# Kernel tuning notes

Measured on AMD Instinct MI355X. Metric: run time of the kernel, lower is better.

The kernel has to match this reference:

```python
import jax, jax.numpy as jnp
import numpy as np

D_MODEL = 2048
N_HEADS = 32
N_KV_HEADS = 8
HEAD_DIM = D_MODEL // N_HEADS  # 64
THETA = 10000.0
BATCH = 2
SEQ = 2048


def _rope_tables(seq_len, head_dim, theta):
    idx = jnp.arange(0, head_dim, 2, dtype=jnp.float32)
    inv_freq = 1.0 / (theta ** (idx / head_dim))
    pos = jnp.arange(seq_len, dtype=jnp.float32)
    angles = pos[:, None] * inv_freq[None, :]  # (S, head_dim/2)
    return jnp.cos(angles), jnp.sin(angles)


def _apply_rope(x, cos, sin):
    # x: (B, H, S, Dh); cos/sin: (S, Dh/2)
    c = cos[None, None, :, :]
    s = sin[None, None, :, :]
    x_even = x[..., 0::2]
    x_odd = x[..., 1::2]
    out_even = x_even * c - x_odd * s
    out_odd = x_even * s + x_odd * c
    # interleave back: stack on last axis and reshape
    return jnp.stack([out_even, out_odd], axis=-1).reshape(x.shape)


def setup_inputs() -> dict:
    key = jax.random.key(0)
    kx, kq, kk, kv, ko = jax.random.split(key, 5)
    std_sq = (2.0 / (D_MODEL + D_MODEL)) ** 0.5
    std_kv = (2.0 / (D_MODEL + N_KV_HEADS * HEAD_DIM)) ** 0.5
    return {
        "x": jax.random.normal(kx, (BATCH, SEQ, D_MODEL), dtype=jnp.float32),
        "Wq": jax.random.normal(kq, (D_MODEL, D_MODEL), dtype=jnp.float32) * std_sq,
        "Wk": jax.random.normal(kk, (N_KV_HEADS * HEAD_DIM, D_MODEL), dtype=jnp.float32) * std_kv,
        "Wv": jax.random.normal(kv, (N_KV_HEADS * HEAD_DIM, D_MODEL), dtype=jnp.float32) * std_kv,
        "Wo": jax.random.normal(ko, (D_MODEL, D_MODEL), dtype=jnp.float32) * std_sq,
    }


def reference(x, Wq, Wk, Wv, Wo):
    B, S, D = x.shape
    groups = N_HEADS // N_KV_HEADS
    cos, sin = _rope_tables(S, HEAD_DIM, THETA)

    q = (x @ Wq.T).reshape(B, S, N_HEADS, HEAD_DIM).transpose(0, 2, 1, 3)
    k = (x @ Wk.T).reshape(B, S, N_KV_HEADS, HEAD_DIM).transpose(0, 2, 1, 3)
    v = (x @ Wv.T).reshape(B, S, N_KV_HEADS, HEAD_DIM).transpose(0, 2, 1, 3)

    q = _apply_rope(q, cos, sin)
    k = _apply_rope(k, cos, sin)

    # GQA: repeat kv heads (repeat_interleave along head dim)
    k = jnp.repeat(k, groups, axis=1)  # (B, H, S, Dh)
    v = jnp.repeat(v, groups, axis=1)

    scale = 1.0 / jnp.sqrt(jnp.float32(HEAD_DIM))
    scores = jnp.einsum('bhqd,bhkd->bhqk', q, k) * scale
    causal = jnp.tril(jnp.ones((S, S), dtype=bool))
    scores = jnp.where(causal[None, None, :, :], scores, -jnp.inf)
    attn = jax.nn.softmax(scores, axis=-1)
    out = jnp.einsum('bhqk,bhkd->bhqd', attn, v)
    out = out.transpose(0, 2, 1, 3).reshape(B, S, D)
    return out @ Wo.T
```

## Files before the change

### kernel.cpp

```cpp
#include <hip/hip_runtime.h>
#include <math.h>

#define BATCHN 2
#define SEQ 2048
#define DMODEL 2048
#define NH 32
#define NKV 8
#define HDIM 64
#define KVD 512
#define ROWS 4096

typedef __bf16 bf16x8 __attribute__((ext_vector_type(8)));
typedef float f32x4 __attribute__((ext_vector_type(4)));
typedef unsigned short u16x8 __attribute__((ext_vector_type(8)));

#define MFMA(a, b, c) __builtin_amdgcn_mfma_f32_16x16x32_bf16(a, b, c, 0, 0, 0)

__device__ __forceinline__ unsigned short f2bf(float f) {
  union { float f; unsigned u; } v; v.f = f;
  unsigned u = v.u;
  u += 0x7fffu + ((u >> 16) & 1u);
  return (unsigned short)(u >> 16);
}

__device__ __forceinline__ unsigned cvtpk(float a, float b) {
  unsigned r;
  asm("v_cvt_pk_bf16_f32 %0, %1, %2" : "=v"(r) : "v"(a), "v"(b));
  return r;
}
__device__ __forceinline__ void pl32(unsigned& a, unsigned& b) {
  asm("v_permlane32_swap_b32 %0, %1" : "+v"(a), "+v"(b));
}
__device__ __forceinline__ void pl16(unsigned& a, unsigned& b) {
  asm("v_permlane16_swap_b32 %0, %1" : "+v"(a), "+v"(b));
}
__device__ __forceinline__ float exp2v(float x) {
  float r;
  asm("v_exp_f32 %0, %1" : "=v"(r) : "v"(x));
  return r;
}

__device__ __forceinline__ void gload16(const void* g, void* l) {
  __builtin_amdgcn_global_load_lds((const __attribute__((address_space(1))) unsigned int*)g,
                                   (__attribute__((address_space(3))) unsigned int*)l, 16, 0, 0);
}

#define FENCE() asm volatile("" ::: "memory")
#define BARRIER() do { FENCE(); __builtin_amdgcn_s_barrier(); FENCE(); } while (0)
#define VMCNT(n) asm volatile("s_waitcnt vmcnt(" #n ")" ::: "memory")

__global__ __launch_bounds__(256) void conv_all(const float* __restrict__ x,
                                                const float* __restrict__ Wq,
                                                const float* __restrict__ Wk,
                                                const float* __restrict__ Wv,
                                                const float* __restrict__ Wo,
                                                unsigned short* __restrict__ xb,
                                                unsigned short* __restrict__ Wqb,
                                                unsigned short* __restrict__ Wkb,
                                                unsigned short* __restrict__ Wvb,
                                                unsigned short* __restrict__ Wob,
                                                float* __restrict__ ct,
                                                float* __restrict__ st) {
  int i = blockIdx.x * 256 + threadIdx.x;
  const float* in;
  unsigned short* out;
  int off;
  if (i < 2097152)      { in = x;  out = xb;  off = i; }
  else if (i < 3145728) { in = Wq; out = Wqb; off = i - 2097152; }
  else if (i < 3407872) { in = Wk; out = Wkb; off = i - 3145728; }
  else if (i < 3670016) { in = Wv; out = Wvb; off = i - 3407872; }
  else if (i < 4718592) { in = Wo; out = Wob; off = i - 3670016; }
  else {
    int t = i - 4718592;
    int s = t >> 5, f = t & 31;
    float inv = __expf(-(float)f * (9.210340371976184f / 32.0f));
    float ang = (float)s * inv;
    ct[t] = cosf(ang);
    st[t] = sinf(ang);
    return;
  }
  float4 v = ((const float4*)in)[off];
  ushort4 o;
  o.x = f2bf(v.x); o.y = f2bf(v.y); o.z = f2bf(v.z); o.w = f2bf(v.w);
  ((ushort4*)out)[off] = o;
}

__global__ __launch_bounds__(512, 2) void gemm_qkv384(const unsigned short* __restrict__ A,
                                                      const unsigned short* __restrict__ Bq,
                                                      const unsigned short* __restrict__ Bk,
                                                      const unsigned short* __restrict__ Bv,
                                                      unsigned short* __restrict__ Qo,
                                                      unsigned short* __restrict__ Ko,
                                                      unsigned short* __restrict__ Vt,
                                                      const float* __restrict__ ct,
                                                      const float* __restrict__ st) {
  __shared__ __align__(16) unsigned short Als[3][8192];
  __shared__ __align__(16) unsigned short Bls[3][2][8192];
  const int tid = threadIdx.x, lane = tid & 63, wv = tid >> 6;
  const int wm = wv >> 2, wn = wv & 3;
  const int g = lane >> 4, r15 = lane & 15;
  const int c = blockIdx.x & 7, i = blockIdx.x >> 3;
  const int bm = (c >> 1) * 8 + (i & 7);
  const int grp = (c & 1) * 4 + (i >> 3);
  const int row0 = bm << 7;
  const unsigned short* Bpan[3];
  int bnp[3];
#pragma unroll
  for (int bk = 0; bk < 3; ++bk) {
    int p = grp * 3 + bk;
    bnp[bk] = p;
    Bpan[bk] = (p < 16) ? Bq + (size_t)(p << 7) * DMODEL
             : (p < 20) ? Bk + (size_t)((p - 16) << 7) * DMODEL
                        : Bv + (size_t)((p - 20) << 7) * DMODEL;
  }
  const int srow = tid >> 3;
  const int scol = (((tid & 7) ^ ((tid >> 3) & 7)) << 3);
  const unsigned short* gA = A + (size_t)(row0 + srow) * DMODEL + scol;
  const unsigned short* gB0 = Bpan[0] + (size_t)srow * DMODEL + scol;
  const unsigned short* gB1 = Bpan[1] + (size_t)srow * DMODEL + scol;
  const unsigned short* gB2 = Bpan[2] + (size_t)srow * DMODEL + scol;

  f32x4 acc[4][6];
#pragma unroll
  for (int a = 0; a < 4; ++a)
#pragma unroll
    for (int b = 0; b < 6; ++b) acc[a][b] = (f32x4){0.f, 0.f, 0.f, 0.f};

#define STG_A(buf, kt) do { \
    gload16(gA + (size_t)(kt) * 64, &Als[buf][(wv << 9)]); \
    gload16(gA + (size_t)64 * DMODEL + (size_t)(kt) * 64, &Als[buf][4096 + (wv << 9)]); } while (0)
#define STG_B(bank, gp, buf, kt) do { \
    gload16(gp + (size_t)(kt) * 64, &Bls[bank][buf][(wv << 9)]); \
    gload16(gp + (size_t)64 * DMODEL + (size_t)(kt) * 64, &Bls[bank][buf][4096 + (wv << 9)]); } while (0)
#define RA(buf, mf, kk) (*(const bf16x8*)&Als[buf][((wm << 6) + ((mf) << 4) + r15) * 64 + \
                          (((((kk) << 2) + g) ^ (r15 & 7)) << 3)])
#define RB(bank, buf, sub, kk) (*(const bf16x8*)&Bls[bank][buf][((wn << 5) + ((sub) << 4) + r15) * 64 + \
                          (((((kk) << 2) + g) ^ (r15 & 7)) << 3)])

  STG_A(0, 0);
  STG_B(0, gB0, 0, 0); STG_B(1, gB1, 0, 0); STG_B(2, gB2, 0, 0);
  STG_A(1, 1);
  VMCNT(0);
  BARRIER();

  const int NT = DMODEL / 64;
  for (int t = 0; t < NT; ++t) {
    const int ab = t % 3, an2 = (t + 2) % 3;
    const int bb = t & 1, bn2 = bb ^ 1;
    bf16x8 af[4][2];
#pragma unroll
    for (int mf = 0; mf < 4; ++mf) { af[mf][0] = RA(ab, mf, 0); af[mf][1] = RA(ab, mf, 1); }
    bf16x8 b01[2][2][2];
#pragma unroll
    for (int bk = 0; bk < 2; ++bk)
#pragma unroll
      for (int sub = 0; sub < 2; ++sub) {
        b01[bk][sub][0] = RB(bk, bb, sub, 0);
        b01[bk][sub][1] = RB(bk, bb, sub, 1);
      }
    if (t + 1 < NT) {
      STG_B(0, gB0, bn2, t + 1); STG_B(1, gB1, bn2, t + 1); STG_B(2, gB2, bn2, t + 1);
    }
    BARRIER();
    __builtin_amdgcn_s_setprio(1);
#pragma unroll
    for (int mf = 0; mf < 4; ++mf)
#pragma unroll
      for (int bk = 0; bk < 2; ++bk)
#pragma unroll
        for (int sub = 0; sub < 2; ++sub) {
          acc[mf][bk * 2 + sub] = MFMA(af[mf][0], b01[bk][sub][0], acc[mf][bk * 2 + sub]);
          acc[mf][bk * 2 + sub] = MFMA(af[mf][1], b01[bk][sub][1], acc[mf][bk * 2 + sub]);
        }
    __builtin_amdgcn_s_setprio(0);
    BARRIER();
    bf16x8 b2[2][2];
#pragma unroll
    for (int sub = 0; sub < 2; ++sub) { b2[sub][0] = RB(2, bb, sub, 0); b2[sub][1] = RB(2, bb, sub, 1); }
    if (t + 2 < NT) STG_A(an2, t + 2);
    BARRIER();
    __builtin_amdgcn_s_setprio(1);
#pragma unroll
    for (int mf = 0; mf < 4; ++mf)
#pragma unroll
      for (int sub = 0; sub < 2; ++sub) {
        acc[mf][4 + sub] = MFMA(af[mf][0], b2[sub][0], acc[mf][4 + sub]);
        acc[mf][4 + sub] = MFMA(af[mf][1], b2[sub][1], acc[mf][4 + sub]);
      }
    __builtin_amdgcn_s_setprio(0);
    if (t + 2 < NT)      { VMCNT(2); }
    else if (t + 1 < NT) { VMCNT(0); }
    BARRIER();
  }
#undef STG_A
#undef STG_B
#undef RA
#undef RB

  const float QS = 0.18033688011112042f;
#pragma unroll
  for (int bk = 0; bk < 3; ++bk) {
    const int p = bnp[bk];
    if (p < 20) {
      unsigned short* Outb = (p < 16) ? Qo : Ko;
      const int col0 = (p < 16) ? (p << 7) : ((p - 16) << 7);
      const int ldo = (p < 16) ? DMODEL : KVD;
      const int qsc = (p < 16);
#pragma unroll
      for (int mf = 0; mf < 4; ++mf) {
#pragma unroll
        for (int rr = 0; rr < 4; ++rr) {
          const int m = row0 + (wm << 6) + (mf << 4) + (g << 2) + rr;
          const float* ctr = ct + ((m & (SEQ - 1)) << 5);
          const float* str = st + ((m & (SEQ - 1)) << 5);
#pragma unroll
          for (int sub = 0; sub < 2; ++sub) {
            const int n = col0 + (wn << 5) + (sub << 4) + r15;
            float v = acc[mf][bk * 2 + sub][rr];
            float pv = __shfl_xor(v, 1);
            int fi = (n & 63) >> 1;
            float cc = ctr[fi], sn = str[fi];
            v = (lane & 1) ? (pv * sn + v * cc) : (v * cc - pv * sn);
            if (qsc) v *= QS;
            Outb[(size_t)m * ldo + n] = f2bf(v);
          }
        }
      }
    } else {
      const int col0 = (p - 20) << 7;
#pragma unroll
      for (int mf = 0; mf < 4; ++mf) {
        const int m0 = row0 + (wm << 6) + (mf << 4) + (g << 2);
        const int b = m0 >> 11, s0 = m0 & (SEQ - 1);
#pragma unroll
        for (int sub = 0; sub < 2; ++sub) {
          const int nv = col0 + (wn << 5) + (sub << 4) + r15;
          ushort4 o;
          o.x = f2bf(acc[mf][bk * 2 + sub][0]);
          o.y = f2bf(acc[mf][bk * 2 + sub][1]);
          o.z = f2bf(acc[mf][bk * 2 + sub][2]);
          o.w = f2bf(acc[mf][bk * 2 + sub][3]);
          *(ushort4*)(Vt + ((size_t)(b * NKV * HDIM + nv)) * SEQ + s0) = o;
        }
      }
    }
  }
}

__global__ __launch_bounds__(512) void gemm_out128(const unsigned short* __restrict__ A,
                                                   const unsigned short* __restrict__ B,
                                                   float* __restrict__ C) {
  __shared__ __align__(16) unsigned short Als[3][8192];
  __shared__ __align__(16) unsigned short Bls[3][2][8192];
  const int tid = threadIdx.x, lane = tid & 63, wv = tid >> 6;
  const int wm = wv >> 2, wn = wv & 3;
  const int g = lane >> 4, r15 = lane & 15;
  const int wgid = (blockIdx.x & 7) * 32 + (blockIdx.x >> 3);
  const int bm = wgid >> 3, bn = wgid & 7;
  const int row0 = bm << 7, col0 = bn << 8;
  const int srl = tid >> 3;
  const int sgc = ((tid & 7) ^ (srl & 7)) << 3;
  const unsigned short* gA = A + (size_t)(row0 + srl) * DMODEL + sgc;
  const unsigned short* gB = B + (size_t)(col0 + srl) * DMODEL + sgc;

  f32x4 acc[4][4];
#pragma unroll
  for (int i = 0; i < 4; ++i)
#pragma unroll
    for (int jj = 0; jj < 4; ++jj) acc[i][jj] = (f32x4){0.f, 0.f, 0.f, 0.f};

#define STG_A1(buf, kt) do { \
    gload16(gA + (size_t)(kt) * 64, &Als[buf][(wv << 9)]); \
    gload16(gA + (size_t)64 * DMODEL + (size_t)(kt) * 64, &Als[buf][4096 + (wv << 9)]); } while (0)
#define STG_B1(buf, h, kt) do { \
    gload16(gB + (size_t)((h) * 128) * DMODEL + (kt) * 64, &Bls[buf][h][(wv << 9)]); \
    gload16(gB + (size_t)((h) * 128 + 64) * DMODEL + (kt) * 64, &Bls[buf][h][4096 + (wv << 9)]); } while (0)
#define RA1(buf, mf, kk) (*(const bf16x8*)&Als[buf][((wm << 6) + (mf) * 16 + r15) * 64 + \
                           (((((kk) << 2) + g) ^ (r15 & 7)) << 3)])
#define RB1(buf, nf, kk) (*(const bf16x8*)&Bls[buf][wn >> 1][((wn & 1) * 64 + (nf) * 16 + r15) * 64 + \
                           (((((kk) << 2) + g) ^ (r15 & 7)) << 3)])

  STG_B1(0, 0, 0); STG_B1(0, 1, 0); STG_A1(0, 0);
  STG_B1(1, 0, 1); STG_B1(1, 1, 1); STG_A1(1, 1);
  VMCNT(6);
  BARRIER();

  const int NT = DMODEL / 64;
  for (int t = 0; t < NT; ++t) {
    const int cur = t % 3;
    const int stg = (t + 2) % 3;
    bf16x8 a[4][2], b0[2][2], b2[2][2];
#pragma unroll
    for (int mf = 0; mf < 4; ++mf) { a[mf][0] = RA1(cur, mf, 0); a[mf][1] = RA1(cur, mf, 1); }
#pragma unroll
    for (int nf = 0; nf < 2; ++nf) { b0[nf][0] = RB1(cur, nf, 0); b0[nf][1] = RB1(cur, nf, 1); }
#pragma unroll
    for (int nf = 0; nf < 2; ++nf) { b2[nf][0] = RB1(cur, 2 + nf, 0); b2[nf][1] = RB1(cur, 2 + nf, 1); }
    if (t + 2 < NT) { STG_B1(stg, 0, t + 2); STG_B1(stg, 1, t + 2); STG_A1(stg, t + 2); }
    BARRIER();
    __builtin_amdgcn_s_setprio(1);
#pragma unroll
    for (int mf = 0; mf < 4; ++mf)
#pragma unroll
      for (int nf = 0; nf < 2; ++nf) {
        acc[mf][nf] = MFMA(a[mf][0], b0[nf][0], acc[mf][nf]);
        acc[mf][nf] = MFMA(a[mf][1], b0[nf][1], acc[mf][nf]);
        acc[mf][2 + nf] = MFMA(a[mf][0], b2[nf][0], acc[mf][2 + nf]);
        acc[mf][2 + nf] = MFMA(a[mf][1], b2[nf][1], acc[mf][2 + nf]);
      }
    __builtin_amdgcn_s_setprio(0);
    if (t + 2 < NT) { VMCNT(6); }
    else if (t + 2 == NT) { VMCNT(0); }
    BARRIER();
  }
#undef STG_A1
#undef STG_B1
#undef RA1
#undef RB1

#pragma unroll
  for (int mf = 0; mf < 4; ++mf)
#pragma unroll
    for (int rr = 0; rr < 4; ++rr) {
      const int m = row0 + (wm << 6) + (mf) * 16 + (g << 2) + rr;
#pragma unroll
      for (int nf = 0; nf < 4; ++nf)
        C[(size_t)m * DMODEL + col0 + (wn << 6) + (nf << 4) + r15] = acc[mf][nf][rr];
    }
}

__global__ __launch_bounds__(512) void attn_fwd(const unsigned short* __restrict__ Q,
                                                const unsigned short* __restrict__ K,
                                                const unsigned short* __restrict__ Vt,
                                                unsigned short* __restrict__ O) {
  __shared__ __align__(16) unsigned short Kls[2][2][64 * 64];
  __shared__ __align__(16) unsigned short Vls[2][2][64 * 64];
  const int bid = blockIdx.x;
  const int xcd = bid & 7;
  const int within = bid >> 3;
  const int grp = xcd * 2 + (within >> 5);
  const int w32 = within & 31;
  const int j = w32 & 7;
  const int hsub = w32 >> 3;
  const int b = grp >> 3, kvh = grp & 7;
  const int h = kvh * 4 + hsub;
  const int wave = threadIdx.x >> 6, lane = threadIdx.x & 63;
  const int g = lane >> 4, r15 = lane & 15;
  const int sr = lane >> 3;
  const int sc = (((lane & 7) << 4) ^ (sr << 4)) >> 1;
  const unsigned short* kbase = K + (size_t)b * SEQ * KVD + kvh * HDIM;
  const unsigned short* vbase = Vt + (size_t)((b * NKV + kvh) * HDIM) * SEQ;

  union { u16x8 s; bf16x8 v; } one8;
#pragma unroll
  for (int z = 0; z < 8; ++z) one8.s[z] = 0x3F80;

  auto STAGE = [&](int bi, int kbv) {
    const int r = wave * 8;
#pragma unroll
    for (int hh = 0; hh < 2; ++hh) {
      gload16(kbase + (size_t)(kbv + hh * 64 + r + sr) * KVD + sc, &Kls[bi][hh][r * 64]);
      gload16(vbase + (size_t)(r + sr) * SEQ + kbv + hh * 64 + sc, &Vls[bi][hh][r * 64]);
    }
  };

#pragma unroll 1
  for (int sel = 0; sel < 2; ++sel) {
    const int qt = sel ? (15 - j) : j;
    const int qrow0 = qt * 128 + wave * 16;
    const unsigned short* qp = Q + (size_t)(b * SEQ + qrow0 + r15) * DMODEL + h * HDIM;
    bf16x8 q0 = *(const bf16x8*)(qp + g * 8);
    bf16x8 q1 = *(const bf16x8*)(qp + 32 + g * 8);
    f32x4 oacc[4] = {};
    f32x4 lacc = {};
    const int kend = (qt + 1) * 128;
    __syncthreads();
    STAGE(0, 0);
    int buf = 0;
    for (int kb = 0; kb < kend; kb += 128) {
      __syncthreads();
      if (kb + 128 < kend) STAGE(buf ^ 1, kb + 128);
#pragma unroll
      for (int hh = 0; hh < 2; ++hh) {
        const char* Kc = (const char*)&Kls[buf][hh][0];
        const char* Vc = (const char*)&Vls[buf][hh][0];
        const int cb = kb + hh * 64;
        f32x4 s[4];
        __builtin_amdgcn_s_setprio(1);
#pragma unroll
        for (int f = 0; f < 4; ++f) {
          const int r = f * 16 + r15;
          const int sw = (r & 7) << 4;
          bf16x8 k0 = *(const bf16x8*)(Kc + r * 128 + ((g * 16) ^ sw));
          bf16x8 k1 = *(const bf16x8*)(Kc + r * 128 + ((64 + g * 16) ^ sw));
          f32x4 z = {};
          s[f] = MFMA(k1, q1, MFMA(k0, q0, z));
        }
        __builtin_amdgcn_s_setprio(0);
        if (cb + 64 > qrow0) {
          const int q = qrow0 + r15;
#pragma unroll
          for (int f = 0; f < 4; ++f)
#pragma unroll
            for (int rr = 0; rr < 4; ++rr)
              if (cb + f * 16 + g * 4 + rr > q) s[f][rr] = -1e30f;
        }
#pragma unroll
        for (int f = 0; f < 4; ++f)
#pragma unroll
          for (int rr = 0; rr < 4; ++rr) s[f][rr] = exp2v(s[f][rr]);
        bf16x8 p1, p2;
        {
          union { bf16x8 v; unsigned u[4]; } P1, P2;
          unsigned a0 = cvtpk(s[0][0], s[0][1]), b0 = cvtpk(s[1][0], s[1][1]);
          pl32(a0, b0); pl16(a0, b0);
          unsigned a1 = cvtpk(s[0][2], s[0][3]), b1 = cvtpk(s[1][2], s[1][3]);
          pl32(a1, b1); pl16(a1, b1);
          P1.u[0] = a0; P1.u[1] = a1; P1.u[2] = b0; P1.u[3] = b1;
          unsigned a2 = cvtpk(s[2][0], s[2][1]), b2 = cvtpk(s[3][0], s[3][1]);
          pl32(a2, b2); pl16(a2, b2);
          unsigned a3 = cvtpk(s[2][2], s[2][3]), b3 = cvtpk(s[3][2], s[3][3]);
          pl32(a3, b3); pl16(a3, b3);
          P2.u[0] = a2; P2.u[1] = a3; P2.u[2] = b2; P2.u[3] = b3;
          p1 = P1.v; p2 = P2.v;
        }
        lacc = MFMA(p2, one8.v, MFMA(p1, one8.v, lacc));
        __builtin_amdgcn_s_setprio(1);
#pragma unroll
        for (int dc = 0; dc < 4; ++dc) {
          const int r = dc * 16 + r15;
          const int sw = (r & 7) << 4;
          bf16x8 v0 = *(const bf16x8*)(Vc + r * 128 + ((g * 16) ^ sw));
          bf16x8 v1 = *(const bf16x8*)(Vc + r * 128 + ((64 + g * 16) ^ sw));
          oacc[dc] = MFMA(p2, v1, MFMA(p1, v0, oacc[dc]));
        }
        __builtin_amdgcn_s_setprio(0);
      }
      buf ^= 1;
    }
    float rls[4];
#pragma unroll
    for (int rr = 0; rr < 4; ++rr) rls[rr] = 1.0f / lacc[rr];
    unsigned short* optr = O + (size_t)(b * SEQ + qrow0) * DMODEL + h * HDIM;
#pragma unroll
    for (int dc = 0; dc < 4; ++dc)
#pragma unroll
      for (int rr = 0; rr < 4; ++rr)
        optr[(size_t)(g * 4 + rr) * DMODEL + dc * 16 + r15] = f2bf(oacc[dc][rr] * rls[rr]);
  }
}

extern "C" void kernel_launch(void* const* d_in, const int* in_sizes, int n_in,
                              void* d_out, int out_size, void* d_ws, size_t ws_size,
                              hipStream_t stream) {
  const float* x  = (const float*)d_in[0];
  const float* Wq = (const float*)d_in[1];
  const float* Wk = (const float*)d_in[2];
  const float* Wv = (const float*)d_in[3];
  const float* Wo = (const float*)d_in[4];

  char* ws = (char*)d_ws;
  unsigned short* xb  = (unsigned short*)(ws);
  unsigned short* Wqb = (unsigned short*)(ws + (16u << 20));
  unsigned short* Wkb = (unsigned short*)(ws + (24u << 20));
  unsigned short* Wvb = (unsigned short*)(ws + (26u << 20));
  unsigned short* Wob = (unsigned short*)(ws + (28u << 20));
  unsigned short* Qb  = (unsigned short*)(ws + (36u << 20));
  unsigned short* Kb  = (unsigned short*)(ws + (52u << 20));
  unsigned short* Vtb = (unsigned short*)(ws + (60u << 20));
  unsigned short* AO  = (unsigned short*)(ws + (64u << 20));
  float* ct = (float*)(ws + (80u << 20));
  float* st = (float*)(ws + (81u << 20));

  conv_all<<<18688, 256, 0, stream>>>(x, Wq, Wk, Wv, Wo, xb, Wqb, Wkb, Wvb, Wob, ct, st);

  gemm_qkv384<<<256, 512, 0, stream>>>(xb, Wqb, Wkb, Wvb, Qb, Kb, Vtb, ct, st);

  attn_fwd<<<512, 512, 0, stream>>>(Qb, Kb, Vtb, AO);

  gemm_out128<<<256, 512, 0, stream>>>(AO, Wob, (float*)d_out);
}
```

Baseline: 159.0 us.

## Process two 16-row query tiles per wave in attention to reuse K/V loads

```diff
diff --git a/kernel.cpp b/kernel.cpp
--- a/kernel.cpp
+++ b/kernel.cpp
@@ -329,19 +329,19 @@
     }
 }
 
-__global__ __launch_bounds__(512) void attn_fwd(const unsigned short* __restrict__ Q,
-                                                const unsigned short* __restrict__ K,
-                                                const unsigned short* __restrict__ Vt,
-                                                unsigned short* __restrict__ O) {
+__global__ __launch_bounds__(512, 2) void attn_fwd(const unsigned short* __restrict__ Q,
+                                                   const unsigned short* __restrict__ K,
+                                                   const unsigned short* __restrict__ Vt,
+                                                   unsigned short* __restrict__ O) {
   __shared__ __align__(16) unsigned short Kls[2][2][64 * 64];
   __shared__ __align__(16) unsigned short Vls[2][2][64 * 64];
   const int bid = blockIdx.x;
   const int xcd = bid & 7;
   const int within = bid >> 3;
-  const int grp = xcd * 2 + (within >> 5);
-  const int w32 = within & 31;
-  const int j = w32 & 7;
-  const int hsub = w32 >> 3;
+  const int grp = xcd * 2 + (within >> 4);
+  const int w16 = within & 15;
+  const int j = w16 & 3;
+  const int hsub = w16 >> 2;
   const int b = grp >> 3, kvh = grp & 7;
   const int h = kvh * 4 + hsub;
   const int wave = threadIdx.x >> 6, lane = threadIdx.x & 63;
@@ -366,14 +366,17 @@
 
 #pragma unroll 1
   for (int sel = 0; sel < 2; ++sel) {
-    const int qt = sel ? (15 - j) : j;
-    const int qrow0 = qt * 128 + wave * 16;
-    const unsigned short* qp = Q + (size_t)(b * SEQ + qrow0 + r15) * DMODEL + h * HDIM;
-    bf16x8 q0 = *(const bf16x8*)(qp + g * 8);
-    bf16x8 q1 = *(const bf16x8*)(qp + 32 + g * 8);
-    f32x4 oacc[4] = {};
-    f32x4 lacc = {};
-    const int kend = (qt + 1) * 128;
+    const int qt = sel ? (7 - j) : j;
+    const int qrow0 = qt * 256 + wave * 32;
+    const unsigned short* qpA = Q + (size_t)(b * SEQ + qrow0 + r15) * DMODEL + h * HDIM;
+    const unsigned short* qpB = qpA + (size_t)16 * DMODEL;
+    bf16x8 qA0 = *(const bf16x8*)(qpA + g * 8);
+    bf16x8 qA1 = *(const bf16x8*)(qpA + 32 + g * 8);
+    bf16x8 qB0 = *(const bf16x8*)(qpB + g * 8);
+    bf16x8 qB1 = *(const bf16x8*)(qpB + 32 + g * 8);
+    f32x4 oA[4] = {}, oB[4] = {};
+    f32x4 lA = {}, lB = {};
+    const int kend = (qt + 1) * 256;
     __syncthreads();
     STAGE(0, 0);
     int buf = 0;
@@ -385,7 +388,7 @@
         const char* Kc = (const char*)&Kls[buf][hh][0];
         const char* Vc = (const char*)&Vls[buf][hh][0];
         const int cb = kb + hh * 64;
-        f32x4 s[4];
+        f32x4 sA[4], sB[4];
         __builtin_amdgcn_s_setprio(1);
 #pragma unroll
         for (int f = 0; f < 4; ++f) {
@@ -393,8 +396,9 @@
           const int sw = (r & 7) << 4;
           bf16x8 k0 = *(const bf16x8*)(Kc + r * 128 + ((g * 16) ^ sw));
           bf16x8 k1 = *(const bf16x8*)(Kc + r * 128 + ((64 + g * 16) ^ sw));
-          f32x4 z = {};
-          s[f] = MFMA(k1, q1, MFMA(k0, q0, z));
+          f32x4 zA = {}, zB = {};
+          sA[f] = MFMA(k1, qA1, MFMA(k0, qA0, zA));
+          sB[f] = MFMA(k1, qB1, MFMA(k0, qB0, zB));
         }
         __builtin_amdgcn_s_setprio(0);
         if (cb + 64 > qrow0) {
@@ -403,28 +407,56 @@
           for (int f = 0; f < 4; ++f)
 #pragma unroll
             for (int rr = 0; rr < 4; ++rr)
-              if (cb + f * 16 + g * 4 + rr > q) s[f][rr] = -1e30f;
+              if (cb + f * 16 + g * 4 + rr > q) sA[f][rr] = -1e30f;
         }
 #pragma unroll
         for (int f = 0; f < 4; ++f)
 #pragma unroll
-          for (int rr = 0; rr < 4; ++rr) s[f][rr] = exp2v(s[f][rr]);
-        bf16x8 p1, p2;
+          for (int rr = 0; rr < 4; ++rr) sA[f][rr] = exp2v(sA[f][rr]);
+        bf16x8 pA1, pA2;
         {
           union { bf16x8 v; unsigned u[4]; } P1, P2;
-          unsigned a0 = cvtpk(s[0][0], s[0][1]), b0 = cvtpk(s[1][0], s[1][1]);
+          unsigned a0 = cvtpk(sA[0][0], sA[0][1]), b0 = cvtpk(sA[1][0], sA[1][1]);
           pl32(a0, b0); pl16(a0, b0);
-          unsigned a1 = cvtpk(s[0][2], s[0][3]), b1 = cvtpk(s[1][2], s[1][3]);
+          unsigned a1 = cvtpk(sA[0][2], sA[0][3]), b1 = cvtpk(sA[1][2], sA[1][3]);
           pl32(a1, b1); pl16(a1, b1);
           P1.u[0] = a0; P1.u[1] = a1; P1.u[2] = b0; P1.u[3] = b1;
-          unsigned a2 = cvtpk(s[2][0], s[2][1]), b2 = cvtpk(s[3][0], s[3][1]);
+          unsigned a2 = cvtpk(sA[2][0], sA[2][1]), b2 = cvtpk(sA[3][0], sA[3][1]);
           pl32(a2, b2); pl16(a2, b2);
-          unsigned a3 = cvtpk(s[2][2], s[2][3]), b3 = cvtpk(s[3][2], s[3][3]);
+          unsigned a3 = cvtpk(sA[2][2], sA[2][3]), b3 = cvtpk(sA[3][2], sA[3][3]);
           pl32(a3, b3); pl16(a3, b3);
           P2.u[0] = a2; P2.u[1] = a3; P2.u[2] = b2; P2.u[3] = b3;
-          p1 = P1.v; p2 = P2.v;
-        }
-        lacc = MFMA(p2, one8.v, MFMA(p1, one8.v, lacc));
+          pA1 = P1.v; pA2 = P2.v;
+        }
+        lA = MFMA(pA2, one8.v, MFMA(pA1, one8.v, lA));
+        if (cb + 64 > qrow0 + 16) {
+          const int q = qrow0 + 16 + r15;
+#pragma unroll
+          for (int f = 0; f < 4; ++f)
+#pragma unroll
+            for (int rr = 0; rr < 4; ++rr)
+              if (cb + f * 16 + g * 4 + rr > q) sB[f][rr] = -1e30f;
+        }
+#pragma unroll
+        for (int f = 0; f < 4; ++f)
+#pragma unroll
+          for (int rr = 0; rr < 4; ++rr) sB[f][rr] = exp2v(sB[f][rr]);
+        bf16x8 pB1, pB2;
+        {
+          union { bf16x8 v; unsigned u[4]; } P1, P2;
+          unsigned a0 = cvtpk(sB[0][0], sB[0][1]), b0 = cvtpk(sB[1][0], sB[1][1]);
+          pl32(a0, b0); pl16(a0, b0);
+          unsigned a1 = cvtpk(sB[0][2], sB[0][3]), b1 = cvtpk(sB[1][2], sB[1][3]);
+          pl32(a1, b1); pl16(a1, b1);
+          P1.u[0] = a0; P1.u[1] = a1; P1.u[2] = b0; P1.u[3] = b1;
+          unsigned a2 = cvtpk(sB[2][0], sB[2][1]), b2 = cvtpk(sB[3][0], sB[3][1]);
+          pl32(a2, b2); pl16(a2, b2);
+          unsigned a3 = cvtpk(sB[2][2], sB[2][3]), b3 = cvtpk(sB[3][2], sB[3][3]);
+          pl32(a3, b3); pl16(a3, b3);
+          P2.u[0] = a2; P2.u[1] = a3; P2.u[2] = b2; P2.u[3] = b3;
+          pB1 = P1.v; pB2 = P2.v;
+        }
+        lB = MFMA(pB2, one8.v, MFMA(pB1, one8.v, lB));
         __builtin_amdgcn_s_setprio(1);
 #pragma unroll
         for (int dc = 0; dc < 4; ++dc) {
@@ -432,21 +464,35 @@
           const int sw = (r & 7) << 4;
           bf16x8 v0 = *(const bf16x8*)(Vc + r * 128 + ((g * 16) ^ sw));
           bf16x8 v1 = *(const bf16x8*)(Vc + r * 128 + ((64 + g * 16) ^ sw));
-          oacc[dc] = MFMA(p2, v1, MFMA(p1, v0, oacc[dc]));
+          oA[dc] = MFMA(pA2, v1, MFMA(pA1, v0, oA[dc]));
+          oB[dc] = MFMA(pB2, v1, MFMA(pB1, v0, oB[dc]));
         }
         __builtin_amdgcn_s_setprio(0);
       }
       buf ^= 1;
     }
-    float rls[4];
-#pragma unroll
-    for (int rr = 0; rr < 4; ++rr) rls[rr] = 1.0f / lacc[rr];
-    unsigned short* optr = O + (size_t)(b * SEQ + qrow0) * DMODEL + h * HDIM;
-#pragma unroll
-    for (int dc = 0; dc < 4; ++dc)
-#pragma unroll
-      for (int rr = 0; rr < 4; ++rr)
-        optr[(size_t)(g * 4 + rr) * DMODEL + dc * 16 + r15] = f2bf(oacc[dc][rr] * rls[rr]);
+    {
+      float rls[4];
+#pragma unroll
+      for (int rr = 0; rr < 4; ++rr) rls[rr] = 1.0f / lA[rr];
+      unsigned short* optr = O + (size_t)(b * SEQ + qrow0) * DMODEL + h * HDIM;
+#pragma unroll
+      for (int dc = 0; dc < 4; ++dc)
+#pragma unroll
+        for (int rr = 0; rr < 4; ++rr)
+          optr[(size_t)(g * 4 + rr) * DMODEL + dc * 16 + r15] = f2bf(oA[dc][rr] * rls[rr]);
+    }
+    {
+      float rls[4];
+#pragma unroll
+      for (int rr = 0; rr < 4; ++rr) rls[rr] = 1.0f / lB[rr];
+      unsigned short* optr = O + (size_t)(b * SEQ + qrow0 + 16) * DMODEL + h * HDIM;
+#pragma unroll
+      for (int dc = 0; dc < 4; ++dc)
+#pragma unroll
+        for (int rr = 0; rr < 4; ++rr)
+          optr[(size_t)(g * 4 + rr) * DMODEL + dc * 16 + r15] = f2bf(oB[dc][rr] * rls[rr]);
+    }
   }
 }
 
@@ -476,7 +522,7 @@
 
   gemm_qkv384<<<256, 512, 0, stream>>>(xb, Wqb, Wkb, Wvb, Qb, Kb, Vtb, ct, st);
 
-  attn_fwd<<<512, 512, 0, stream>>>(Qb, Kb, Vtb, AO);
+  attn_fwd<<<256, 512, 0, stream>>>(Qb, Kb, Vtb, AO);
 
   gemm_out128<<<256, 512, 0, stream>>>(AO, Wob, (float*)d_out);
 }
```

Measured after the change: 162.4 us. 1.02x slower.
